# Kernel tuning notes

Hardware: AMD Instinct MI355X
Metric: run time of the kernel (lower is better)

The kernel has to match this reference:

```python
import jax, jax.numpy as jnp
import numpy as np


def setup_inputs() -> dict:
    key = jax.random.key(0)
    k1, k2 = jax.random.split(key)
    B, N, D = 32, 8192, 64
    x = jax.random.normal(k1, (B, N, D), dtype=jnp.float32)
    y = jax.random.normal(k2, (B, D, N), dtype=jnp.float32)
    return {"x": x, "y": y}


def reference(x, y):
    # Original: full cdist [B,N,N], mean over batch, take diagonal.
    # Only matched pairs (i,i) survive, so compute them directly —
    # mathematically identical output and gradients.
    y_t = jnp.transpose(y, (0, 2, 1))          # [B, N, D]
    diff = x - y_t                             # [B, N, D]
    pair_dist = jnp.sqrt(jnp.sum(diff * diff, axis=-1))  # [B, N]
    dist_diag = jnp.mean(pair_dist, axis=0)    # [N] == diag(mean_b cdist)
    dist_diag = dist_diag.at[1:3].multiply(1.5)
    loss = jnp.mean(dist_diag)
    return loss
```

## Files before the change

kernel.cpp:

```cpp
#include <hip/hip_runtime.h>


constexpr int B  = 32;
constexpr int N  = 8192;
constexpr int D  = 64;
constexpr int TN = 64;
constexpr int NBLK = (N / TN) * B;

#define GLD_LDS(gp, lp, sz)                                                              \
    __builtin_amdgcn_global_load_lds(                                                    \
        (const __attribute__((address_space(1))) void*)(gp),                             \
        (__attribute__((address_space(3))) void*)(lp), (sz), 0, 0)

__global__ __launch_bounds__(256) void euclid_loss_kernel(
    const float* __restrict__ x,
    const float* __restrict__ y,
    float* __restrict__ ws)
{
    __shared__ float x_s[TN * D];
    __shared__ float y_s[D * TN];

    const int tid  = threadIdx.x;
    const int wave = tid >> 6;
    const int lane = tid & 63;
    const int n0   = blockIdx.x * TN;
    const int b    = blockIdx.y;

    const float* xg = x + ((size_t)b * N + n0) * D;
    const float* yg = y + (size_t)b * D * N + n0;

#pragma unroll
    for (int j = 0; j < 4; ++j) {
        const int c = wave * 4 + j;
        GLD_LDS(xg + c * 256 + lane * 4, x_s + c * 256, 16);
    }
#pragma unroll
    for (int j = 0; j < 16; ++j) {
        const int d = wave * 16 + j;
        GLD_LDS(yg + (size_t)d * N + lane, y_s + d * TN, 4);
    }

    __syncthreads();

    float acc = 0.0f;
#pragma unroll
    for (int s = 0; s < 16; ++s) {
        const int d  = wave * 16 + ((lane + s) & 15);
        const float df = x_s[lane * D + d] - y_s[d * TN + lane];
        acc += df * df;
    }

    __syncthreads();
    x_s[wave * TN + lane] = acc;
    __syncthreads();

    if (tid < TN) {
        const float s = x_s[tid] + x_s[TN + tid] + x_s[2 * TN + tid] + x_s[3 * TN + tid];
        const int   n = n0 + tid;
        const float w = (n == 1 || n == 2) ? 1.5f : 1.0f;
        float v = w * __builtin_sqrtf(s);
#pragma unroll
        for (int off = 32; off > 0; off >>= 1) v += __shfl_down(v, off, 64);
        if (tid == 0)
            ws[blockIdx.y * gridDim.x + blockIdx.x] = v;
    }
}

__global__ __launch_bounds__(256) void reduce_kernel(
    const float* __restrict__ ws,
    float* __restrict__ out)
{
    const int tid = threadIdx.x;
    float v = 0.0f;
#pragma unroll
    for (int j = 0; j < NBLK / (256 * 4); ++j) {
        const float4 p = *reinterpret_cast<const float4*>(ws + j * 1024 + tid * 4);
        v += p.x + p.y + p.z + p.w;
    }
#pragma unroll
    for (int off = 32; off > 0; off >>= 1) v += __shfl_down(v, off, 64);

    __shared__ float wsum[4];
    if ((tid & 63) == 0) wsum[tid >> 6] = v;
    __syncthreads();
    if (tid == 0)
        out[0] = (wsum[0] + wsum[1] + wsum[2] + wsum[3]) * (1.0f / (float)(B * N));
}

extern "C" void kernel_launch(void* const* d_in, const int* in_sizes, int n_in,
                              void* d_out, int out_size, void* d_ws, size_t ws_size,
                              hipStream_t stream) {
    const float* x = (const float*)d_in[0];
    const float* y = (const float*)d_in[1];
    float* out = (float*)d_out;
    float* ws  = (float*)d_ws;

    dim3 grid(N / TN, B);
    euclid_loss_kernel<<<grid, 256, 0, stream>>>(x, y, ws);
    reduce_kernel<<<1, 256, 0, stream>>>(ws, out);
}
```

Baseline: 141.9 us.

## Load x directly to registers and widen y LDS loads to 16 bytes

Each thread now loads its row slice of x straight into registers with float4 loads instead of staging it through LDS, which frees that LDS buffer and drops a barrier. The y tile is still staged in LDS, but through 16-byte global_load_lds transfers (four per wave) instead of sixteen 4-byte ones. The aim is fewer load instructions, less LDS traffic and footprint, and better occupancy. The trade-off is that the direct x loads are strided per lane (each lane reads 64 bytes of its own row), so coalescing depends on cache-line reuse across the four waves.

```diff
diff --git a/kernel.cpp b/kernel.cpp
--- a/kernel.cpp
+++ b/kernel.cpp
@@ -7,18 +7,18 @@
 constexpr int TN = 64;
 constexpr int NBLK = (N / TN) * B;
 
-#define GLD_LDS(gp, lp, sz)                                                              \
+#define GLD_LDS16(gp, lp)                                                                \
     __builtin_amdgcn_global_load_lds(                                                    \
         (const __attribute__((address_space(1))) void*)(gp),                             \
-        (__attribute__((address_space(3))) void*)(lp), (sz), 0, 0)
+        (__attribute__((address_space(3))) void*)(lp), 16, 0, 0)
 
 __global__ __launch_bounds__(256) void euclid_loss_kernel(
     const float* __restrict__ x,
     const float* __restrict__ y,
     float* __restrict__ ws)
 {
-    __shared__ float x_s[TN * D];
     __shared__ float y_s[D * TN];
+    __shared__ float part[4][TN];
 
     const int tid  = threadIdx.x;
     const int wave = tid >> 6;
@@ -26,36 +26,38 @@
     const int n0   = blockIdx.x * TN;
     const int b    = blockIdx.y;
 
-    const float* xg = x + ((size_t)b * N + n0) * D;
     const float* yg = y + (size_t)b * D * N + n0;
+#pragma unroll
+    for (int i = 0; i < 4; ++i) {
+        const int d0 = wave * 16 + i * 4;
+        const float* gsrc = yg + (size_t)(d0 + (lane >> 4)) * N + (lane & 15) * 4;
+        GLD_LDS16(gsrc, y_s + d0 * TN);
+    }
 
+    const float* xp = x + ((size_t)b * N + n0 + lane) * D + wave * 16;
+    float4 xv[4];
 #pragma unroll
-    for (int j = 0; j < 4; ++j) {
-        const int c = wave * 4 + j;
-        GLD_LDS(xg + c * 256 + lane * 4, x_s + c * 256, 16);
-    }
-#pragma unroll
-    for (int j = 0; j < 16; ++j) {
-        const int d = wave * 16 + j;
-        GLD_LDS(yg + (size_t)d * N + lane, y_s + d * TN, 4);
-    }
+    for (int j = 0; j < 4; ++j)
+        xv[j] = *reinterpret_cast<const float4*>(xp + 4 * j);
 
     __syncthreads();
 
     float acc = 0.0f;
 #pragma unroll
-    for (int s = 0; s < 16; ++s) {
-        const int d  = wave * 16 + ((lane + s) & 15);
-        const float df = x_s[lane * D + d] - y_s[d * TN + lane];
-        acc += df * df;
+    for (int j = 0; j < 4; ++j) {
+        const int d = wave * 16 + j * 4;
+        const float d0 = xv[j].x - y_s[(d + 0) * TN + lane];
+        const float d1 = xv[j].y - y_s[(d + 1) * TN + lane];
+        const float d2 = xv[j].z - y_s[(d + 2) * TN + lane];
+        const float d3 = xv[j].w - y_s[(d + 3) * TN + lane];
+        acc += d0 * d0 + d1 * d1 + d2 * d2 + d3 * d3;
     }
 
-    __syncthreads();
-    x_s[wave * TN + lane] = acc;
+    part[wave][lane] = acc;
     __syncthreads();
 
     if (tid < TN) {
-        const float s = x_s[tid] + x_s[TN + tid] + x_s[2 * TN + tid] + x_s[3 * TN + tid];
+        const float s = part[0][tid] + part[1][tid] + part[2][tid] + part[3][tid];
         const int   n = n0 + tid;
         const float w = (n == 1 || n == 2) ? 1.5f : 1.0f;
         float v = w * __builtin_sqrtf(s);
```

New measurement: 143.0 us. About the same (+0.8%).
